# Kernel tuning notes

Hardware: AMD Instinct MI355X
Metric: run time of the kernel (lower is better)

The kernel has to match this reference:

```python
import jax, jax.numpy as jnp
import numpy as np


def setup_inputs() -> dict:
    key = jax.random.key(0)
    ks = jax.random.split(key, 8)
    B, C, H, W = 4, 512, 64, 64
    O = 64  # output_size for f/g projections
    x = jax.random.normal(ks[0], (B, C, H, W), dtype=jnp.float32)
    s = 0.02
    f_w = jax.random.normal(ks[1], (O, C), dtype=jnp.float32) * s
    f_b = jnp.zeros((O,), dtype=jnp.float32)
    g_w = jax.random.normal(ks[2], (O, C), dtype=jnp.float32) * s
    g_b = jnp.zeros((O,), dtype=jnp.float32)
    h_w = jax.random.normal(ks[3], (C, C), dtype=jnp.float32) * s
    h_b = jnp.zeros((C,), dtype=jnp.float32)
    gamma = jnp.float32(0.5)  # torch init is 0.0; nonzero to exercise the attention path
    return {"x": x, "f_w": f_w, "f_b": f_b, "g_w": g_w, "g_b": g_b,
            "h_w": h_w, "h_b": h_b, "gamma": gamma}


def reference(x, f_w, f_b, g_w, g_b, h_w, h_b, gamma):
    B, C, Hh, Ww = x.shape
    N = Hh * Ww
    # 1x1 convs == per-pixel linear projections
    xf = x.reshape(B, C, N)                                   # [B,C,N]
    f = jnp.einsum('oc,bcn->bon', f_w, xf) + f_b[None, :, None]  # [B,O,N]
    g = jnp.einsum('oc,bcn->bon', g_w, xf) + g_b[None, :, None]  # [B,O,N]
    h = jnp.einsum('oc,bcn->bon', h_w, xf) + h_b[None, :, None]  # [B,C,N]
    # scores[b,i,j] = <f[:, i], g[:, j]>  (f transposed to [B,N,O] then bmm with g)
    scores = jnp.einsum('boi,boj->bij', f, g)                 # [B,N,N]
    # NOTE: original uses nn.Softmax(dim=1) -> normalize over the i (first N) axis
    sm = jax.nn.softmax(scores, axis=1)                       # [B,N,N]
    attn = jnp.einsum('bcn,bnm->bcm', h, sm)                  # [B,C,N]
    out = gamma * attn.reshape(B, C, Hh, Ww) + x
    return out
```

## Files before the change

### kernel.cpp

```cpp
#include <hip/hip_runtime.h>


#define N_PIX 4096
#define C_IN  512

typedef __attribute__((ext_vector_type(8)))  short bf16x8;
typedef __attribute__((ext_vector_type(16))) float f32x16;
typedef __attribute__((ext_vector_type(8)))  int   i32x8;

__device__ __forceinline__ float fexp2(float x) {
    return __builtin_amdgcn_exp2f(x);
}

__device__ inline unsigned int f2bf(float f) {
    union { float f; unsigned u; } x; x.f = f;
    unsigned r = x.u + 0x7FFFu + ((x.u >> 16) & 1u);
    return r >> 16;
}

__device__ __forceinline__ unsigned cvt_pk_bf16(float a, float b) {
#if __has_builtin(__builtin_amdgcn_cvt_pk_bf16_f32)
    auto r = __builtin_amdgcn_cvt_pk_bf16_f32(a, b);
    unsigned u; __builtin_memcpy(&u, &r, 4); return u;
#else
    return f2bf(a) | (f2bf(b) << 16);
#endif
}

__device__ __forceinline__ unsigned pk_fp8x4(float a, float b, float c, float d) {
    int v = 0;
    v = __builtin_amdgcn_cvt_pk_fp8_f32(a, b, v, false);
    v = __builtin_amdgcn_cvt_pk_fp8_f32(c, d, v, true);
    return (unsigned)v;
}

#define RAW_BARRIER() do { \
    __builtin_amdgcn_sched_barrier(0); \
    asm volatile("s_waitcnt lgkmcnt(0)" ::: "memory"); \
    __builtin_amdgcn_s_barrier(); \
    __builtin_amdgcn_sched_barrier(0); \
} while (0)

__global__ __launch_bounds__(256) void pack_w(
    const float* __restrict__ f_w, const float* __restrict__ g_w,
    const float* __restrict__ h_w, unsigned short* __restrict__ wall)
{
    __shared__ __align__(16) unsigned short Ls[32 * 520];
    const int t  = threadIdx.x;
    const int tt = blockIdx.x;
    const float* W; int rbase;
    if (tt < 2)      { W = f_w; rbase = tt * 32; }
    else if (tt < 4) { W = g_w; rbase = (tt - 2) * 32; }
    else             { W = h_w; rbase = (tt - 4) * 32; }
    const float fs = (tt < 2) ? 1.442695041f : 1.0f;

    #pragma unroll
    for (int k = 0; k < 16; ++k) {
        const int off = (t + k * 256) * 4;
        const int row = off >> 9, col = off & 511;
        float4 v = *(const float4*)&W[(size_t)(rbase + row) * C_IN + col];
        uint2 pk; pk.x = cvt_pk_bf16(v.x * fs, v.y * fs); pk.y = cvt_pk_bf16(v.z * fs, v.w * fs);
        *(uint2*)&Ls[row * 520 + col] = pk;
    }
    __syncthreads();
    #pragma unroll
    for (int j = 0; j < 8; ++j) {
        const int o = t + j * 256;
        const int q = o >> 6, lq = o & 63;
        const int row = lq & 31, c0 = q * 16 + (lq >> 5) * 8;
        uint4 pk = *(const uint4*)&Ls[row * 520 + c0];
        *(uint4*)&wall[(size_t)tt * 16384 + (size_t)o * 8] = pk;
    }
}

__global__ __launch_bounds__(512, 2) void proj_kernel(
    const float* __restrict__ x,
    const unsigned short* __restrict__ wall,
    const float* __restrict__ f_b, const float* __restrict__ g_b,
    const float* __restrict__ h_b,
    unsigned short* __restrict__ fa, unsigned short* __restrict__ gbuf,
    unsigned char* __restrict__ ha)
{
    __shared__ __align__(16) unsigned short Xf[2][4096];
    const int t    = threadIdx.x;
    const int w    = t >> 6;
    const int l    = t & 63;
    const int half = l >> 5;
    const int tx = t & 15;
    const int ty = t >> 4;
    const int c0 = ty * 2;
    const int qs = c0 >> 4;
    const int woff = (c0 & 7);
    const int hfs = (c0 >> 3) & 1;

    const int blk = blockIdx.x;

    if (blk < 256) {
        const int b  = blk >> 6;
        const int nb = blk & 63;
        const int n0g = nb * 64;
        const int n0 = tx * 4;

        f32x16 acc[2][2];
        #pragma unroll
        for (int j = 0; j < 2; ++j)
            #pragma unroll
            for (int s = 0; s < 2; ++s)
                #pragma unroll
                for (int r = 0; r < 16; ++r) acc[j][s][r] = 0.f;

        const unsigned short* wp0 = wall + (size_t)(4 + w * 2) * 16384 + (size_t)l * 8;
        const unsigned short* wp1 = wp0 + 16384;
        bf16x8 wc0 = *(const bf16x8*)wp0;
        bf16x8 wc1 = *(const bf16x8*)wp1;

        float4 v0 = *(const float4*)&x[((size_t)(b * C_IN + c0)) * N_PIX + n0g + n0];
        float4 v1 = *(const float4*)&x[((size_t)(b * C_IN + c0 + 1)) * N_PIX + n0g + n0];

        for (int it = 0; it < 8; ++it) {
            {
                unsigned short* xb = &Xf[it & 1][0];
                const float a0[4] = {v0.x, v0.y, v0.z, v0.w};
                const float a1[4] = {v1.x, v1.y, v1.z, v1.w};
                #pragma unroll
                for (int j = 0; j < 4; ++j) {
                    const int n = n0 + j;
                    const int off = ((n >> 5) * 4 + qs) * 512
                                  + ((n & 31) + 32 * hfs) * 8 + woff;
                    *(unsigned*)&xb[off] = cvt_pk_bf16(a0[j], a1[j]);
                }
            }
            if (it < 7) {
                v0 = *(const float4*)&x[((size_t)(b * C_IN + (it + 1) * 64 + c0)) * N_PIX + n0g + n0];
                v1 = *(const float4*)&x[((size_t)(b * C_IN + (it + 1) * 64 + c0 + 1)) * N_PIX + n0g + n0];
            }
            RAW_BARRIER();
            const unsigned short* xb = &Xf[it & 1][0];
            #pragma unroll
            for (int q = 0; q < 4; ++q) {
                const int qn = (it * 4 + q + 1) & 31;
                bf16x8 wn0 = *(const bf16x8*)(wp0 + (size_t)qn * 512);
                bf16x8 wn1 = *(const bf16x8*)(wp1 + (size_t)qn * 512);
                bf16x8 x0 = *(const bf16x8*)&xb[(0 * 4 + q) * 512 + l * 8];
                bf16x8 x1 = *(const bf16x8*)&xb[(1 * 4 + q) * 512 + l * 8];
                acc[0][0] = __builtin_amdgcn_mfma_f32_32x32x16_bf16(x0, wc0, acc[0][0], 0, 0, 0);
                acc[0][1] = __builtin_amdgcn_mfma_f32_32x32x16_bf16(x1, wc0, acc[0][1], 0, 0, 0);
                acc[1][0] = __builtin_amdgcn_mfma_f32_32x32x16_bf16(x0, wc1, acc[1][0], 0, 0, 0);
                acc[1][1] = __builtin_amdgcn_mfma_f32_32x32x16_bf16(x1, wc1, acc[1][1], 0, 0, 0);
                wc0 = wn0; wc1 = wn1;
            }
        }

        const int nt_ = nb >> 1, kt_ = nb & 1;
        #pragma unroll
        for (int j = 0; j < 2; ++j) {
            const int ctile = w * 2 + j;
            const int ch = ctile * 32 + (l & 31);
            const float hb = h_b[ch];
            unsigned char* hdst = ha
                + (((size_t)(b * 16 + ctile) * 32 + nt_) * 2 + kt_) * 2048
                + (size_t)(l & 31) * 32 + 16 * half;
            #pragma unroll
            for (int ns = 0; ns < 2; ++ns) {
                uint4 pk4;
                pk4.x = pk_fp8x4(acc[j][ns][0]  + hb, acc[j][ns][1]  + hb,
                                 acc[j][ns][2]  + hb, acc[j][ns][3]  + hb);
                pk4.y = pk_fp8x4(acc[j][ns][4]  + hb, acc[j][ns][5]  + hb,
                                 acc[j][ns][6]  + hb, acc[j][ns][7]  + hb);
                pk4.z = pk_fp8x4(acc[j][ns][8]  + hb, acc[j][ns][9]  + hb,
                                 acc[j][ns][10] + hb, acc[j][ns][11] + hb);
                pk4.w = pk_fp8x4(acc[j][ns][12] + hb, acc[j][ns][13] + hb,
                                 acc[j][ns][14] + hb, acc[j][ns][15] + hb);
                *(uint4*)&hdst[ns * 1024] = pk4;
            }
        }
    } else {
        const int blk2 = blk - 256;
        const int b   = blk2 >> 6;
        const int nb2 = blk2 & 63;
        const int n0g = nb2 * 64;
        const int n0 = tx * 4;
        const int tt    = w & 3;
        const int npair = w >> 2;

        f32x16 acc;
        #pragma unroll
        for (int r = 0; r < 16; ++r) acc[r] = 0.f;

        const unsigned short* wpf = wall + (size_t)tt * 16384 + (size_t)l * 8;
        bf16x8 wcf = *(const bf16x8*)wpf;

        float4 v0 = *(const float4*)&x[((size_t)(b * C_IN + c0)) * N_PIX + n0g + n0];
        float4 v1 = *(const float4*)&x[((size_t)(b * C_IN + c0 + 1)) * N_PIX + n0g + n0];

        for (int it = 0; it < 8; ++it) {
            {
                unsigned short* xb = &Xf[it & 1][0];
                const float a0[4] = {v0.x, v0.y, v0.z, v0.w};
                const float a1[4] = {v1.x, v1.y, v1.z, v1.w};
                #pragma unroll
                for (int j = 0; j < 4; ++j) {
                    const int n = n0 + j;
                    const int off = ((n >> 5) * 4 + qs) * 512
                                  + ((n & 31) + 32 * hfs) * 8 + woff;
                    *(unsigned*)&xb[off] = cvt_pk_bf16(a0[j], a1[j]);
                }
            }
            if (it < 7) {
                v0 = *(const float4*)&x[((size_t)(b * C_IN + (it + 1) * 64 + c0)) * N_PIX + n0g + n0];
                v1 = *(const float4*)&x[((size_t)(b * C_IN + (it + 1) * 64 + c0 + 1)) * N_PIX + n0g + n0];
            }
            RAW_BARRIER();
            const unsigned short* xb = &Xf[it & 1][0];
            #pragma unroll
            for (int q = 0; q < 4; ++q) {
                const int qn = (it * 4 + q + 1) & 31;
                bf16x8 wnf = *(const bf16x8*)(wpf + (size_t)qn * 512);
                bf16x8 x0 = *(const bf16x8*)&xb[(npair * 4 + q) * 512 + l * 8];
                acc = __builtin_amdgcn_mfma_f32_32x32x16_bf16(wcf, x0, acc, 0, 0, 0);
                wcf = wnf;
            }
        }

        unsigned short* buf = (tt < 2) ? fa : gbuf;
        const float* bias = (tt < 2) ? f_b : g_b;
        const float bscale = (tt < 2) ? 1.442695041f : 1.0f;
        const int ntile = nb2 * 2 + npair;
        #pragma unroll
        for (int j2 = 0; j2 < 4; ++j2) {
            const int o_base = (tt & 1) * 32 + 8 * j2 + 4 * half;
            float4 bv = *(const float4*)&bias[o_base];
            bv.x *= bscale; bv.y *= bscale; bv.z *= bscale; bv.w *= bscale;
            const int q  = o_base >> 4;
            const int lp = (l & 31) + 32 * (j2 & 1);
            uint2 pk;
            pk.x = cvt_pk_bf16(acc[4 * j2 + 0] + bv.x, acc[4 * j2 + 1] + bv.y);
            pk.y = cvt_pk_bf16(acc[4 * j2 + 2] + bv.z, acc[4 * j2 + 3] + bv.w);
            size_t off = (((size_t)(b * 128 + ntile) * 4 + q) * 64 + lp) * 8 + 4 * half;
            *(uint2*)&buf[off] = pk;
        }
    }
}

__global__ __launch_bounds__(1024, 1) void attn_kernel(
    const unsigned short* __restrict__ fa,
    const unsigned short* __restrict__ gbuf,
    const unsigned char* __restrict__ ha,
    const float* __restrict__ x,
    const float* __restrict__ gamma_p,
    float* __restrict__ out)
{
    __shared__ __align__(16) unsigned char Ebuf[2][64 * 136];
    __shared__ float den_part[4][64];
    __shared__ float den_inv[64];

    const int t    = threadIdx.x;
    const int w    = t >> 6;
    const int l    = t & 63;
    const int lane = l & 31;
    const int half = l >> 5;
    const bool prod = (w < 8);
    const int nsub = w & 3;
    const int mt   = w >> 2;

    const int blk = blockIdx.x;
    const int b   = blk & 3;
    const int mi  = blk >> 2;
    const int m0  = mi * 64;
    const int ctg = w;

    f32x16 acc[2];
    #pragma unroll
    for (int j = 0; j < 2; ++j)
        #pragma unroll
        for (int r = 0; r < 16; ++r) acc[j][r] = 0.f;

    float denp = 0.f;

    const unsigned char* hptr = ha
        + (size_t)(b * 16 + ctg) * 131072 + (size_t)l * 32;
    i32x8 h0 = *(const i32x8*)hptr;
    i32x8 h1 = *(const i32x8*)(hptr + 2048);
    hptr += 4096;

    bf16x8 gfrag[4];
    bf16x8 ff[4];
    const unsigned short* fptr = fa + (size_t)b * (128 * 4) * 512
                               + (size_t)(nsub * 4) * 512 + (size_t)l * 8;

    if (prod) {
        const unsigned short* gp = gbuf
            + ((size_t)(b * 128 + mi * 2 + mt) * 4) * 512 + (size_t)l * 8;
        #pragma unroll
        for (int q = 0; q < 4; ++q)
            gfrag[q] = *(const bf16x8*)(gp + (size_t)q * 512);
        #pragma unroll
        for (int q = 0; q < 4; ++q)
            ff[q] = *(const bf16x8*)(fptr + (size_t)q * 512);
        fptr += 8192;

        f32x16 s;
        #pragma unroll
        for (int r = 0; r < 16; ++r) s[r] = 0.f;
        #pragma unroll
        for (int q = 0; q < 4; ++q)
            s = __builtin_amdgcn_mfma_f32_32x32x16_bf16(ff[q], gfrag[q], s, 0, 0, 0);
        #pragma unroll
        for (int q = 0; q < 4; ++q)
            ff[q] = *(const bf16x8*)(fptr + (size_t)q * 512);
        fptr += 8192;
        unsigned pkv[4];
        #pragma unroll
        for (int r4 = 0; r4 < 4; ++r4) {
            float e0 = fexp2(s[r4 * 4 + 0] - 8.656170f);
            float e1 = fexp2(s[r4 * 4 + 1] - 8.656170f);
            float e2 = fexp2(s[r4 * 4 + 2] - 8.656170f);
            float e3 = fexp2(s[r4 * 4 + 3] - 8.656170f);
            denp += (e0 + e1) + (e2 + e3);
            pkv[r4] = pk_fp8x4(e0, e1, e2, e3);
        }
        unsigned char* ew = &Ebuf[0][(mt * 32 + lane) * 136 + nsub * 32 + half * 16];
        *(unsigned long long*)(ew)     = (unsigned long long)pkv[0]
                                       | ((unsigned long long)pkv[1] << 32);
        *(unsigned long long*)(ew + 8) = (unsigned long long)pkv[2]
                                       | ((unsigned long long)pkv[3] << 32);
    }
    RAW_BARRIER();

    for (int nt = 0; nt < 31; ++nt) {
        if (prod) {
            __builtin_amdgcn_s_setprio(1);
            f32x16 s;
            #pragma unroll
            for (int r = 0; r < 16; ++r) s[r] = 0.f;
            #pragma unroll
            for (int q = 0; q < 4; ++q)
                s = __builtin_amdgcn_mfma_f32_32x32x16_bf16(ff[q], gfrag[q], s, 0, 0, 0);
            #pragma unroll
            for (int q = 0; q < 4; ++q)
                ff[q] = *(const bf16x8*)(fptr + (size_t)q * 512);
            fptr += 8192;
            __builtin_amdgcn_s_setprio(0);
            unsigned pkv[4];
            #pragma unroll
            for (int r4 = 0; r4 < 4; ++r4) {
                float e0 = fexp2(s[r4 * 4 + 0] - 8.656170f);
                float e1 = fexp2(s[r4 * 4 + 1] - 8.656170f);
                float e2 = fexp2(s[r4 * 4 + 2] - 8.656170f);
                float e3 = fexp2(s[r4 * 4 + 3] - 8.656170f);
                denp += (e0 + e1) + (e2 + e3);
                pkv[r4] = pk_fp8x4(e0, e1, e2, e3);
            }
            unsigned char* ew = &Ebuf[(nt + 1) & 1][(mt * 32 + lane) * 136 + nsub * 32 + half * 16];
            *(unsigned long long*)(ew)     = (unsigned long long)pkv[0]
                                           | ((unsigned long long)pkv[1] << 32);
            *(unsigned long long*)(ew + 8) = (unsigned long long)pkv[2]
                                           | ((unsigned long long)pkv[3] << 32);
        }

        {
            __builtin_amdgcn_s_setprio(1);
            const unsigned char* eb = &Ebuf[nt & 1][0];
            #pragma unroll
            for (int kt = 0; kt < 2; ++kt) {
                const unsigned char* e0p = eb + lane * 136 + kt * 64 + half * 32;
                union { i32x8 v; long d[4]; } b0, b1;
                #pragma unroll
                for (int j = 0; j < 4; ++j) {
                    b0.d[j] = *(const long*)(e0p + 8 * j);
                    b1.d[j] = *(const long*)(e0p + 32 * 136 + 8 * j);
                }
                const i32x8 av = kt ? h1 : h0;
                acc[0] = __builtin_amdgcn_mfma_scale_f32_32x32x64_f8f6f4(
                    av, b0.v, acc[0], 0, 0, 0, 127, 0, 127);
                acc[1] = __builtin_amdgcn_mfma_scale_f32_32x32x64_f8f6f4(
                    av, b1.v, acc[1], 0, 0, 0, 127, 0, 127);
            }
            __builtin_amdgcn_s_setprio(0);
            h0 = *(const i32x8*)hptr;
            h1 = *(const i32x8*)(hptr + 2048);
            hptr += 4096;
        }

        RAW_BARRIER();
    }

    {
        const unsigned char* eb = &Ebuf[31 & 1][0];
        #pragma unroll
        for (int kt = 0; kt < 2; ++kt) {
            const unsigned char* e0p = eb + lane * 136 + kt * 64 + half * 32;
            union { i32x8 v; long d[4]; } b0, b1;
            #pragma unroll
            for (int j = 0; j < 4; ++j) {
                b0.d[j] = *(const long*)(e0p + 8 * j);
                b1.d[j] = *(const long*)(e0p + 32 * 136 + 8 * j);
            }
            const i32x8 av = kt ? h1 : h0;
            acc[0] = __builtin_amdgcn_mfma_scale_f32_32x32x64_f8f6f4(
                av, b0.v, acc[0], 0, 0, 0, 127, 0, 127);
            acc[1] = __builtin_amdgcn_mfma_scale_f32_32x32x64_f8f6f4(
                av, b1.v, acc[1], 0, 0, 0, 127, 0, 127);
        }
    }

    if (prod) {
        denp += __shfl_xor(denp, 32, 64);
        if (l < 32) den_part[nsub][mt * 32 + lane] = denp;
    }
    __syncthreads();
    if (t < 64) {
        float d = den_part[0][t] + den_part[1][t] + den_part[2][t] + den_part[3][t];
        den_inv[t] = 1.0f / d;
    }
    __syncthreads();

    const float gs = gamma_p[0];
    #pragma unroll
    for (int mt2 = 0; mt2 < 2; ++mt2) {
        const int mloc = mt2 * 32 + lane;
        const float dinv = den_inv[mloc];
        const int m = m0 + mloc;
        #pragma unroll
        for (int r = 0; r < 16; ++r) {
            const int c = ctg * 32 + (r & 3) + ((r >> 2) * 8) + half * 4;
            const size_t idx = ((size_t)(b * C_IN + c)) * N_PIX + m;
            out[idx] = gs * acc[mt2][r] * dinv + x[idx];
        }
    }
}

extern "C" void kernel_launch(void* const* d_in, const int* in_sizes, int n_in,
                              void* d_out, int out_size, void* d_ws, size_t ws_size,
                              hipStream_t stream)
{
    const float* x     = (const float*)d_in[0];
    const float* f_w   = (const float*)d_in[1];
    const float* f_b   = (const float*)d_in[2];
    const float* g_w   = (const float*)d_in[3];
    const float* g_b   = (const float*)d_in[4];
    const float* h_w   = (const float*)d_in[5];
    const float* h_b   = (const float*)d_in[6];
    const float* gamma = (const float*)d_in[7];
    float* out = (float*)d_out;

    unsigned short* fa   = (unsigned short*)d_ws;
    unsigned short* gbuf = fa + (1u << 20);
    unsigned char*  ha   = (unsigned char*)(gbuf + (1u << 20));
    unsigned short* wall = (unsigned short*)(ha + (8u << 20));

    pack_w<<<20, 256, 0, stream>>>(f_w, g_w, h_w, wall);

    proj_kernel<<<512, 512, 0, stream>>>(x, wall, f_b, g_b, h_b, fa, gbuf, ha);

    attn_kernel<<<256, 1024, 0, stream>>>(fa, gbuf, ha, x, gamma, out);
}
```

Baseline: 155.4 us.

## Warp-specialize attention kernel into separate producer and consumer waves

The kernel is split into two roles. Previously all 16 waves ran the fp8 P·H MFMA accumulation and the first 8 also produced the exp scores. Now waves 0-7 only compute scores, exponentials and the denominator. Waves 8-15 only consume the shared-memory E tiles, each handling two 32-channel groups and writing the output. The goal is to stop producer waves stalling on consumer MFMA work, so the two stages overlap more cleanly. In exchange, each consumer wave holds twice the accumulators and H fragments, which raises register pressure, and the workload may be unbalanced between the two roles.

```diff
diff --git a/kernel.cpp b/kernel.cpp
--- a/kernel.cpp
+++ b/kernel.cpp
@@ -267,69 +267,27 @@
     const int b   = blk & 3;
     const int mi  = blk >> 2;
     const int m0  = mi * 64;
-    const int ctg = w;
-
-    f32x16 acc[2];
-    #pragma unroll
-    for (int j = 0; j < 2; ++j)
-        #pragma unroll
-        for (int r = 0; r < 16; ++r) acc[j][r] = 0.f;
 
     float denp = 0.f;
 
-    const unsigned char* hptr = ha
-        + (size_t)(b * 16 + ctg) * 131072 + (size_t)l * 32;
-    i32x8 h0 = *(const i32x8*)hptr;
-    i32x8 h1 = *(const i32x8*)(hptr + 2048);
-    hptr += 4096;
-
-    bf16x8 gfrag[4];
-    bf16x8 ff[4];
-    const unsigned short* fptr = fa + (size_t)b * (128 * 4) * 512
-                               + (size_t)(nsub * 4) * 512 + (size_t)l * 8;
-
     if (prod) {
-        const unsigned short* gp = gbuf
-            + ((size_t)(b * 128 + mi * 2 + mt) * 4) * 512 + (size_t)l * 8;
-        #pragma unroll
-        for (int q = 0; q < 4; ++q)
-            gfrag[q] = *(const bf16x8*)(gp + (size_t)q * 512);
+        bf16x8 gfrag[4];
+        bf16x8 ff[4];
+        const unsigned short* fptr = fa + (size_t)b * (128 * 4) * 512
+                                   + (size_t)(nsub * 4) * 512 + (size_t)l * 8;
+        {
+            const unsigned short* gp = gbuf
+                + ((size_t)(b * 128 + mi * 2 + mt) * 4) * 512 + (size_t)l * 8;
+            #pragma unroll
+            for (int q = 0; q < 4; ++q)
+                gfrag[q] = *(const bf16x8*)(gp + (size_t)q * 512);
+        }
         #pragma unroll
         for (int q = 0; q < 4; ++q)
             ff[q] = *(const bf16x8*)(fptr + (size_t)q * 512);
         fptr += 8192;
 
-        f32x16 s;
-        #pragma unroll
-        for (int r = 0; r < 16; ++r) s[r] = 0.f;
-        #pragma unroll
-        for (int q = 0; q < 4; ++q)
-            s = __builtin_amdgcn_mfma_f32_32x32x16_bf16(ff[q], gfrag[q], s, 0, 0, 0);
-        #pragma unroll
-        for (int q = 0; q < 4; ++q)
-            ff[q] = *(const bf16x8*)(fptr + (size_t)q * 512);
-        fptr += 8192;
-        unsigned pkv[4];
-        #pragma unroll
-        for (int r4 = 0; r4 < 4; ++r4) {
-            float e0 = fexp2(s[r4 * 4 + 0] - 8.656170f);
-            float e1 = fexp2(s[r4 * 4 + 1] - 8.656170f);
-            float e2 = fexp2(s[r4 * 4 + 2] - 8.656170f);
-            float e3 = fexp2(s[r4 * 4 + 3] - 8.656170f);
-            denp += (e0 + e1) + (e2 + e3);
-            pkv[r4] = pk_fp8x4(e0, e1, e2, e3);
-        }
-        unsigned char* ew = &Ebuf[0][(mt * 32 + lane) * 136 + nsub * 32 + half * 16];
-        *(unsigned long long*)(ew)     = (unsigned long long)pkv[0]
-                                       | ((unsigned long long)pkv[1] << 32);
-        *(unsigned long long*)(ew + 8) = (unsigned long long)pkv[2]
-                                       | ((unsigned long long)pkv[3] << 32);
-    }
-    RAW_BARRIER();
-
-    for (int nt = 0; nt < 31; ++nt) {
-        if (prod) {
-            __builtin_amdgcn_s_setprio(1);
+        {
             f32x16 s;
             #pragma unroll
             for (int r = 0; r < 16; ++r) s[r] = 0.f;
@@ -340,7 +298,6 @@
             for (int q = 0; q < 4; ++q)
                 ff[q] = *(const bf16x8*)(fptr + (size_t)q * 512);
             fptr += 8192;
-            __builtin_amdgcn_s_setprio(0);
             unsigned pkv[4];
             #pragma unroll
             for (int r4 = 0; r4 < 4; ++r4) {
@@ -351,14 +308,74 @@
                 denp += (e0 + e1) + (e2 + e3);
                 pkv[r4] = pk_fp8x4(e0, e1, e2, e3);
             }
+            unsigned char* ew = &Ebuf[0][(mt * 32 + lane) * 136 + nsub * 32 + half * 16];
+            *(unsigned long long*)(ew)     = (unsigned long long)pkv[0]
+                                           | ((unsigned long long)pkv[1] << 32);
+            *(unsigned long long*)(ew + 8) = (unsigned long long)pkv[2]
+                                           | ((unsigned long long)pkv[3] << 32);
+        }
+        RAW_BARRIER();
+
+        for (int nt = 0; nt < 31; ++nt) {
+            __builtin_amdgcn_s_setprio(1);
+            f32x16 s;
+            #pragma unroll
+            for (int r = 0; r < 16; ++r) s[r] = 0.f;
+            #pragma unroll
+            for (int q = 0; q < 4; ++q)
+                s = __builtin_amdgcn_mfma_f32_32x32x16_bf16(ff[q], gfrag[q], s, 0, 0, 0);
+            #pragma unroll
+            for (int q = 0; q < 4; ++q)
+                ff[q] = *(const bf16x8*)(fptr + (size_t)q * 512);
+            fptr += 8192;
+            __builtin_amdgcn_s_setprio(0);
+            unsigned pkv[4];
+            #pragma unroll
+            for (int r4 = 0; r4 < 4; ++r4) {
+                float e0 = fexp2(s[r4 * 4 + 0] - 8.656170f);
+                float e1 = fexp2(s[r4 * 4 + 1] - 8.656170f);
+                float e2 = fexp2(s[r4 * 4 + 2] - 8.656170f);
+                float e3 = fexp2(s[r4 * 4 + 3] - 8.656170f);
+                denp += (e0 + e1) + (e2 + e3);
+                pkv[r4] = pk_fp8x4(e0, e1, e2, e3);
+            }
             unsigned char* ew = &Ebuf[(nt + 1) & 1][(mt * 32 + lane) * 136 + nsub * 32 + half * 16];
             *(unsigned long long*)(ew)     = (unsigned long long)pkv[0]
                                            | ((unsigned long long)pkv[1] << 32);
             *(unsigned long long*)(ew + 8) = (unsigned long long)pkv[2]
                                            | ((unsigned long long)pkv[3] << 32);
-        }
-
-        {
+            RAW_BARRIER();
+        }
+
+        denp += __shfl_xor(denp, 32, 64);
+        if (l < 32) den_part[nsub][mt * 32 + lane] = denp;
+        __syncthreads();
+        if (t < 64) {
+            float d = den_part[0][t] + den_part[1][t] + den_part[2][t] + den_part[3][t];
+            den_inv[t] = 1.0f / d;
+        }
+        __syncthreads();
+    } else {
+        const int cw  = w - 8;
+        const int cA  = cw * 2;
+        const int cB  = cA + 1;
+        f32x16 accA[2], accB[2];
+        #pragma unroll
+        for (int j = 0; j < 2; ++j)
+            #pragma unroll
+            for (int r = 0; r < 16; ++r) { accA[j][r] = 0.f; accB[j][r] = 0.f; }
+
+        const unsigned char* hpA = ha + (size_t)(b * 16 + cA) * 131072 + (size_t)l * 32;
+        const unsigned char* hpB = ha + (size_t)(b * 16 + cB) * 131072 + (size_t)l * 32;
+        i32x8 hA0 = *(const i32x8*)hpA;
+        i32x8 hA1 = *(const i32x8*)(hpA + 2048);
+        i32x8 hB0 = *(const i32x8*)hpB;
+        i32x8 hB1 = *(const i32x8*)(hpB + 2048);
+        hpA += 4096; hpB += 4096;
+
+        RAW_BARRIER();
+
+        for (int nt = 0; nt < 31; ++nt) {
             __builtin_amdgcn_s_setprio(1);
             const unsigned char* eb = &Ebuf[nt & 1][0];
             #pragma unroll
@@ -370,62 +387,67 @@
                     b0.d[j] = *(const long*)(e0p + 8 * j);
                     b1.d[j] = *(const long*)(e0p + 32 * 136 + 8 * j);
                 }
-                const i32x8 av = kt ? h1 : h0;
-                acc[0] = __builtin_amdgcn_mfma_scale_f32_32x32x64_f8f6f4(
-                    av, b0.v, acc[0], 0, 0, 0, 127, 0, 127);
-                acc[1] = __builtin_amdgcn_mfma_scale_f32_32x32x64_f8f6f4(
-                    av, b1.v, acc[1], 0, 0, 0, 127, 0, 127);
+                const i32x8 avA = kt ? hA1 : hA0;
+                const i32x8 avB = kt ? hB1 : hB0;
+                accA[0] = __builtin_amdgcn_mfma_scale_f32_32x32x64_f8f6f4(
+                    avA, b0.v, accA[0], 0, 0, 0, 127, 0, 127);
+                accA[1] = __builtin_amdgcn_mfma_scale_f32_32x32x64_f8f6f4(
+                    avA, b1.v, accA[1], 0, 0, 0, 127, 0, 127);
+                accB[0] = __builtin_amdgcn_mfma_scale_f32_32x32x64_f8f6f4(
+                    avB, b0.v, accB[0], 0, 0, 0, 127, 0, 127);
+                accB[1] = __builtin_amdgcn_mfma_scale_f32_32x32x64_f8f6f4(
+                    avB, b1.v, accB[1], 0, 0, 0, 127, 0, 127);
             }
             __builtin_amdgcn_s_setprio(0);
-            h0 = *(const i32x8*)hptr;
-            h1 = *(const i32x8*)(hptr + 2048);
-            hptr += 4096;
-        }
-
-        RAW_BARRIER();
-    }
-
-    {
-        const unsigned char* eb = &Ebuf[31 & 1][0];
-        #pragma unroll
-        for (int kt = 0; kt < 2; ++kt) {
-            const unsigned char* e0p = eb + lane * 136 + kt * 64 + half * 32;
-            union { i32x8 v; long d[4]; } b0, b1;
-            #pragma unroll
-            for (int j = 0; j < 4; ++j) {
-                b0.d[j] = *(const long*)(e0p + 8 * j);
-                b1.d[j] = *(const long*)(e0p + 32 * 136 + 8 * j);
-            }
-            const i32x8 av = kt ? h1 : h0;
-            acc[0] = __builtin_amdgcn_mfma_scale_f32_32x32x64_f8f6f4(
-                av, b0.v, acc[0], 0, 0, 0, 127, 0, 127);
-            acc[1] = __builtin_amdgcn_mfma_scale_f32_32x32x64_f8f6f4(
-                av, b1.v, acc[1], 0, 0, 0, 127, 0, 127);
-        }
-    }
-
-    if (prod) {
-        denp += __shfl_xor(denp, 32, 64);
-        if (l < 32) den_part[nsub][mt * 32 + lane] = denp;
-    }
-    __syncthreads();
-    if (t < 64) {
-        float d = den_part[0][t] + den_part[1][t] + den_part[2][t] + den_part[3][t];
-        den_inv[t] = 1.0f / d;
-    }
-    __syncthreads();
-
-    const float gs = gamma_p[0];
-    #pragma unroll
-    for (int mt2 = 0; mt2 < 2; ++mt2) {
-        const int mloc = mt2 * 32 + lane;
-        const float dinv = den_inv[mloc];
-        const int m = m0 + mloc;
-        #pragma unroll
-        for (int r = 0; r < 16; ++r) {
-            const int c = ctg * 32 + (r & 3) + ((r >> 2) * 8) + half * 4;
-            const size_t idx = ((size_t)(b * C_IN + c)) * N_PIX + m;
-            out[idx] = gs * acc[mt2][r] * dinv + x[idx];
+            hA0 = *(const i32x8*)hpA;
+            hA1 = *(const i32x8*)(hpA + 2048);
+            hB0 = *(const i32x8*)hpB;
+            hB1 = *(const i32x8*)(hpB + 2048);
+            hpA += 4096; hpB += 4096;
+            RAW_BARRIER();
+        }
+
+        {
+            const unsigned char* eb = &Ebuf[31 & 1][0];
+            #pragma unroll
+            for (int kt = 0; kt < 2; ++kt) {
+                const unsigned char* e0p = eb + lane * 136 + kt * 64 + half * 32;
+                union { i32x8 v; long d[4]; } b0, b1;
+                #pragma unroll
+                for (int j = 0; j < 4; ++j) {
+                    b0.d[j] = *(const long*)(e0p + 8 * j);
+                    b1.d[j] = *(const long*)(e0p + 32 * 136 + 8 * j);
+                }
+                const i32x8 avA = kt ? hA1 : hA0;
+                const i32x8 avB = kt ? hB1 : hB0;
+                accA[0] = __builtin_amdgcn_mfma_scale_f32_32x32x64_f8f6f4(
+                    avA, b0.v, accA[0], 0, 0, 0, 127, 0, 127);
+                accA[1] = __builtin_amdgcn_mfma_scale_f32_32x32x64_f8f6f4(
+                    avA, b1.v, accA[1], 0, 0, 0, 127, 0, 127);
+                accB[0] = __builtin_amdgcn_mfma_scale_f32_32x32x64_f8f6f4(
+                    avB, b0.v, accB[0], 0, 0, 0, 127, 0, 127);
+                accB[1] = __builtin_amdgcn_mfma_scale_f32_32x32x64_f8f6f4(
+                    avB, b1.v, accB[1], 0, 0, 0, 127, 0, 127);
+            }
+        }
+
+        __syncthreads();
+        __syncthreads();
+
+        const float gs = gamma_p[0];
+        #pragma unroll
+        for (int mt2 = 0; mt2 < 2; ++mt2) {
+            const int mloc = mt2 * 32 + lane;
+            const float dinv = den_inv[mloc];
+            const int m = m0 + mloc;
+            #pragma unroll
+            for (int r = 0; r < 16; ++r) {
+                const int co = (r & 3) + ((r >> 2) * 8) + half * 4;
+                const size_t idxA = ((size_t)(b * C_IN + cA * 32 + co)) * N_PIX + m;
+                const size_t idxB = ((size_t)(b * C_IN + cB * 32 + co)) * N_PIX + m;
+                out[idxA] = gs * accA[mt2][r] * dinv + x[idxA];
+                out[idxB] = gs * accB[mt2][r] * dinv + x[idxB];
+            }
         }
     }
 }
```

Result: no change. 153.0 us, median of 2 (-1.5%).
